# Kernel optimization log

Measured on AMD Instinct MI355X. Metric: run time of the kernel, lower is better.

The kernel has to match this reference:

```python
import jax, jax.numpy as jnp
import numpy as np

D_MODEL, N_LEVELS, N_HEADS, N_POINTS = 256, 4, 8, 4
HEAD_DIM = D_MODEL // N_HEADS
SPATIAL = [(100, 100), (50, 50), (25, 25), (13, 13)]  # (H, W) per level
BATCH = 2


def setup_inputs() -> dict:
    key = jax.random.key(0)
    ks = jax.random.split(key, 10)
    len_in = sum(h * w for h, w in SPATIAL)
    n, lq = BATCH, len_in
    s = 0.02
    mlp = N_HEADS * N_LEVELS * N_POINTS
    starts = np.cumsum([0] + [h * w for h, w in SPATIAL])[:-1]
    return {
        "query": jax.random.normal(ks[0], (n, lq, D_MODEL), jnp.float32),
        "reference_points": jax.random.uniform(ks[1], (n, lq, N_LEVELS, 2), jnp.float32),
        "input_flatten": jax.random.normal(ks[2], (n, len_in, D_MODEL), jnp.float32),
        "input_spatial_shapes": jnp.array(SPATIAL, dtype=jnp.int32),
        "input_level_start_index": jnp.array(starts, dtype=jnp.int32),
        "Wv": jax.random.normal(ks[3], (D_MODEL, D_MODEL), jnp.float32) * s,
        "bv": jnp.zeros((D_MODEL,), jnp.float32),
        "Woff": jax.random.normal(ks[4], (D_MODEL, mlp * 2), jnp.float32) * s,
        "boff": jax.random.normal(ks[5], (mlp * 2,), jnp.float32) * s,
        "Wattn": jax.random.normal(ks[6], (D_MODEL, mlp), jnp.float32) * s,
        "battn": jnp.zeros((mlp,), jnp.float32),
        "Wout": jax.random.normal(ks[7], (D_MODEL, D_MODEL), jnp.float32) * s,
        "bout": jnp.zeros((D_MODEL,), jnp.float32),
    }


def _ms_deform_attn_core(value, spatial_shapes, loc, aw):
    """value [N,S,M,D]; loc [N,Lq,M,L,P,2] in [0,1]; aw [N,Lq,M,L,P] -> [N,Lq,M*D].
    Faithful to F.grid_sample(mode='bilinear', padding_mode='zeros', align_corners=False)."""
    n, lq, m, L, p, _ = loc.shape
    d = value.shape[-1]
    out = jnp.zeros((n, m, lq, d), value.dtype)
    gather = jax.vmap(jax.vmap(lambda v, i: v[i]))  # vmap over N and M
    start = 0
    for lvl, (H, W) in enumerate(spatial_shapes):
        v = value[:, start:start + H * W].transpose(0, 2, 1, 3)  # [N,M,HW,D]
        start += H * W
        # align_corners=False: grid g=2*loc-1 -> pixel = ((g+1)*size-1)/2 = loc*size-0.5
        x = loc[:, :, :, lvl, :, 0] * W - 0.5  # [N,Lq,M,P]
        y = loc[:, :, :, lvl, :, 1] * H - 0.5
        x0 = jnp.floor(x)
        y0 = jnp.floor(y)
        wx = x - x0
        wy = y - y0
        x0i = x0.astype(jnp.int32)
        y0i = y0.astype(jnp.int32)
        samp = jnp.zeros((n, m, lq * p, d), value.dtype)
        for dy, wyc in ((0, 1.0 - wy), (1, wy)):
            for dx, wxc in ((0, 1.0 - wx), (1, wx)):
                xi = x0i + dx
                yi = y0i + dy
                valid = (xi >= 0) & (xi < W) & (yi >= 0) & (yi < H)  # zeros padding
                idx = jnp.clip(yi, 0, H - 1) * W + jnp.clip(xi, 0, W - 1)
                idx = idx.transpose(0, 2, 1, 3).reshape(n, m, lq * p)
                w = (wxc * wyc * valid).transpose(0, 2, 1, 3).reshape(n, m, lq * p)
                samp = samp + gather(v, idx) * w[..., None]
        samp = samp.reshape(n, m, lq, p, d)
        aw_l = aw[:, :, :, lvl, :].transpose(0, 2, 1, 3)  # [N,M,Lq,P]
        out = out + (samp * aw_l[..., None]).sum(3)
    return out.transpose(0, 2, 1, 3).reshape(n, lq, m * d)


def reference(query, reference_points, input_flatten, input_spatial_shapes,
              input_level_start_index, Wv, bv, Woff, boff, Wattn, battn, Wout, bout):
    n, lq, _ = query.shape
    m, L, p = N_HEADS, N_LEVELS, N_POINTS
    shapes = np.asarray(input_spatial_shapes)  # concrete/static [L,2] = (H,W)
    value = (input_flatten @ Wv + bv).reshape(n, -1, m, HEAD_DIM)
    off = (query @ Woff + boff).reshape(n, lq, m, L, p, 2)
    aw = jax.nn.softmax((query @ Wattn + battn).reshape(n, lq, m, L * p), axis=-1)
    aw = aw.reshape(n, lq, m, L, p)
    norm = jnp.asarray(shapes[:, ::-1].astype(np.float32))  # [L,2] = (W,H)
    loc = reference_points[:, :, None, :, None, :] + off / norm[None, None, None, :, None, :]
    out = _ms_deform_attn_core(value, [tuple(s) for s in shapes.tolist()], loc, aw)
    return out @ Wout + bout
```

## Files before the change

kernel.cpp:

```cpp
#include <hip/hip_runtime.h>
#include <hip/hip_bf16.h>

#define NB    2
#define LQ    13294
#define DM    256
#define NH    8
#define HD    32
#define NL    4
#define NP    4
#define ROWS  (NB*LQ)

#define OFF_VALUE 0u
#define OFF_TMP   13613056u
#define OFF_OFFS  27226112u
#define OFF_AWL   54452224u
#define OFF_WT    61258752u
#define OFF_FLAG  61717504u

#define WT_WV    0
#define WT_WOFF  65536
#define WT_WATTN 131072
#define WT_WOUT  163840

typedef __attribute__((ext_vector_type(8))) short short8;
typedef __attribute__((ext_vector_type(4))) float floatx4;

static __device__ __forceinline__ float blo(int u)  { return __uint_as_float(((unsigned)u) << 16); }
static __device__ __forceinline__ float bhif(int u) { return __uint_as_float(((unsigned)u) & 0xffff0000u); }

static __device__ __forceinline__ int pack_bf2(float a, float b) {
    __hip_bfloat162 h(__float2bfloat16(a), __float2bfloat16(b));
    int u; __builtin_memcpy(&u, &h, 4); return u;
}

static __device__ __forceinline__ float load_bias(const void* b, int i, int flag) {
    return flag ? __bfloat162float(((const __hip_bfloat16*)b)[i]) : ((const float*)b)[i];
}

static __device__ __forceinline__ void gload_lds16(const void* g, void* l) {
    __builtin_amdgcn_global_load_lds(
        (const __attribute__((address_space(1))) unsigned*)g,
        (__attribute__((address_space(3))) unsigned*)l, 16, 0, 0);
}

__global__ void sniff_k(const unsigned int* __restrict__ q, int* __restrict__ flag) {
    const int t = threadIdx.x;
    int hits = 0;
#pragma unroll
    for (int i = 0; i < 4; ++i) {
        unsigned lo = q[t * 4 + i] & 0xffffu;
        unsigned e  = (lo >> 7) & 0xffu;
        if ((e >= 110u && e <= 132u) || lo == 0u) ++hits;
    }
#pragma unroll
    for (int s = 1; s < 64; s <<= 1) hits += __shfl_xor(hits, s);
    if (t == 0) *flag = (hits > 160) ? 1 : 0;
}

__global__ __launch_bounds__(256) void trans_k(
    const void* __restrict__ s0, const void* __restrict__ s1,
    const void* __restrict__ s2, const void* __restrict__ s3,
    short* __restrict__ wt, const int* __restrict__ flagp)
{
    const int flag = *flagp;
    const int z = blockIdx.z;
    const void* src = (z == 0) ? s0 : (z == 1) ? s1 : (z == 2) ? s2 : s3;
    short* dst = wt + ((z == 0) ? WT_WV : (z == 1) ? WT_WOFF : (z == 2) ? WT_WATTN : WT_WOUT);
    const int N = (z == 2) ? 128 : 256;
    const int n0 = blockIdx.x * 32, k0 = blockIdx.y * 32;
    if (n0 >= N) return;

    __shared__ short tile[32 * 36];
    const int t = threadIdx.x;
    const int r = t >> 3, c4 = (t & 7) * 4;
    if (flag) {
        const short* sp = (const short*)src + (k0 + r) * N + n0 + c4;
        *(short4*)&tile[r * 36 + c4] = *(const short4*)sp;
    } else {
        const float* sp = (const float*)src + (k0 + r) * N + n0 + c4;
        float4 v = *(const float4*)sp;
        short4 o;
        o.x = (short)(pack_bf2(v.x, v.x) & 0xffff);
        o.y = (short)(pack_bf2(v.y, v.y) & 0xffff);
        o.z = (short)(pack_bf2(v.z, v.z) & 0xffff);
        o.w = (short)(pack_bf2(v.w, v.w) & 0xffff);
        *(short4*)&tile[r * 36 + c4] = o;
    }
    __syncthreads();
    const int nn = t >> 3, r4 = (t & 7) * 4;
    short4 o;
    o.x = tile[(r4 + 0) * 36 + nn];
    o.y = tile[(r4 + 1) * 36 + nn];
    o.z = tile[(r4 + 2) * 36 + nn];
    o.w = tile[(r4 + 3) * 36 + nn];
    *(short4*)&dst[(n0 + nn) * 256 + k0 + r4] = o;
}

__global__ __launch_bounds__(256) void gemm_front_k(
    const void* __restrict__ flat, const void* __restrict__ query,
    const short* __restrict__ wt,
    const void* __restrict__ bv, const void* __restrict__ boff, const void* __restrict__ battn,
    short* __restrict__ value, float* __restrict__ offsb, short* __restrict__ awl,
    const int* __restrict__ flagp)
{
    const int  flag = *flagp;
    const bool a_bf = (flag != 0);

    __shared__ __align__(16) short Bs[128 * 256];
    __shared__ __align__(16) short As[2][128 * 32];

    const int tid = threadIdx.x;
    const int w = tid >> 6, lane = tid & 63;
    const int qd = lane >> 4, ln = lane & 15;
    const int bx = blockIdx.x;
    const bool isv = (bx < 2);
    const void*  A   = isv ? flat : query;
    const short* Wtb = isv ? (wt + WT_WV) : (wt + WT_WOFF);
    const int colbase = (isv ? bx : bx - 2) * 128;
    const int bm = blockIdx.y * 128;

#pragma unroll
    for (int r = 0; r < 16; ++r) {
        const int c = r * 256 + tid;
        const int col = c >> 5;
        const int kc = (c & 31) ^ (col & 31);
        gload_lds16(Wtb + (colbase + col) * 256 + kc * 8, &Bs[(r * 256 + w * 64) * 8]);
    }

    auto stage_a = [&](int buf, int k0) {
#pragma unroll
        for (int r = 0; r < 2; ++r) {
            const int c = r * 256 + tid;
            const int row = min(bm + (c >> 2), ROWS - 1);
            const int kc = ((c & 3) ^ ((c >> 2) & 3)) * 8;
            if (a_bf) {
                gload_lds16((const short*)A + row * 256 + k0 + kc,
                            &As[buf][(r * 256 + w * 64) * 8]);
            } else {
                const float* p = (const float*)A + row * 256 + k0 + kc;
                float4 f0 = *(const float4*)p, f1 = *(const float4*)(p + 4);
                int4 pk; pk.x = pack_bf2(f0.x, f0.y); pk.y = pack_bf2(f0.z, f0.w);
                         pk.z = pack_bf2(f1.x, f1.y); pk.w = pack_bf2(f1.z, f1.w);
                *(int4*)&As[buf][c * 8] = pk;
            }
        }
    };
    stage_a(0, 0);
    __syncthreads();

    const int wm = (w & 1) * 64, wn = (w >> 1) * 64;

    floatx4 acc[4][4];
#pragma unroll
    for (int i = 0; i < 4; ++i)
#pragma unroll
        for (int j = 0; j < 4; ++j) acc[i][j] = floatx4{0.f, 0.f, 0.f, 0.f};

#pragma unroll
    for (int i0 = 0; i0 < 8; ++i0) {
        if (i0 < 7) stage_a((i0 + 1) & 1, 32 * (i0 + 1));
        const short* Ab = As[i0 & 1];
        short8 af[4], bf[4];
#pragma unroll
        for (int i = 0; i < 4; ++i) {
            const int row = wm + i * 16 + ln;
            af[i] = *(const short8*)&Ab[(row * 4 + (qd ^ (row & 3))) * 8];
        }
#pragma unroll
        for (int j = 0; j < 4; ++j) {
            const int col = wn + j * 16 + ln;
            bf[j] = *(const short8*)&Bs[(col * 32 + ((4 * i0 + qd) ^ (col & 31))) * 8];
        }
#pragma unroll
        for (int i = 0; i < 4; ++i)
#pragma unroll
            for (int j = 0; j < 4; ++j)
                acc[i][j] = __builtin_amdgcn_mfma_f32_16x16x32_bf16(af[i], bf[j], acc[i][j], 0, 0, 0);
        if (i0 < 7) __syncthreads();
    }

#pragma unroll
    for (int j = 0; j < 4; ++j) {
        const int col = colbase + wn + j * 16 + ln;
        float bj;
        if (isv)            bj = load_bias(bv, col, flag);
        else if (col < 256) bj = load_bias(boff, col, flag);
        else                bj = load_bias(battn, col - 256, flag);
#pragma unroll
        for (int i = 0; i < 4; ++i) {
#pragma unroll
            for (int r = 0; r < 4; ++r) {
                const int row = bm + wm + i * 16 + qd * 4 + r;
                if (row >= ROWS) continue;
                const float v = acc[i][j][r] + bj;
                if (isv)            value[row * 256 + col] = (short)(pack_bf2(v, v) & 0xffff);
                else if (col < 256) offsb[row * 256 + col] = v;
                else                awl[row * 128 + col - 256] = (short)(pack_bf2(v, v) & 0xffff);
            }
        }
    }
}

__global__ __launch_bounds__(256) void gemm_out_k(
    const short* __restrict__ tmp, const short* __restrict__ wtout,
    const void* __restrict__ bout, void* __restrict__ C,
    const int* __restrict__ flagp)
{
    const int flag = *flagp;

    __shared__ __align__(16) short Bs[128 * 256];
    __shared__ __align__(16) short As[2][128 * 32];

    const int tid = threadIdx.x;
    const int w = tid >> 6, lane = tid & 63;
    const int qd = lane >> 4, ln = lane & 15;
    const int colbase = blockIdx.x * 128;
    const int bm = blockIdx.y * 128;

#pragma unroll
    for (int r = 0; r < 16; ++r) {
        const int c = r * 256 + tid;
        const int col = c >> 5;
        const int kc = (c & 31) ^ (col & 31);
        gload_lds16(wtout + (colbase + col) * 256 + kc * 8, &Bs[(r * 256 + w * 64) * 8]);
    }

    auto stage_a = [&](int buf, int k0) {
#pragma unroll
        for (int r = 0; r < 2; ++r) {
            const int c = r * 256 + tid;
            const int row = min(bm + (c >> 2), ROWS - 1);
            const int kc = ((c & 3) ^ ((c >> 2) & 3)) * 8;
            gload_lds16(tmp + row * 256 + k0 + kc, &As[buf][(r * 256 + w * 64) * 8]);
        }
    };
    stage_a(0, 0);
    __syncthreads();

    const int wm = (w & 1) * 64, wn = (w >> 1) * 64;

    floatx4 acc[4][4];
#pragma unroll
    for (int i = 0; i < 4; ++i)
#pragma unroll
        for (int j = 0; j < 4; ++j) acc[i][j] = floatx4{0.f, 0.f, 0.f, 0.f};

#pragma unroll
    for (int i0 = 0; i0 < 8; ++i0) {
        if (i0 < 7) stage_a((i0 + 1) & 1, 32 * (i0 + 1));
        const short* Ab = As[i0 & 1];
        short8 af[4], bf[4];
#pragma unroll
        for (int i = 0; i < 4; ++i) {
            const int row = wm + i * 16 + ln;
            af[i] = *(const short8*)&Ab[(row * 4 + (qd ^ (row & 3))) * 8];
        }
#pragma unroll
        for (int j = 0; j < 4; ++j) {
            const int col = wn + j * 16 + ln;
            bf[j] = *(const short8*)&Bs[(col * 32 + ((4 * i0 + qd) ^ (col & 31))) * 8];
        }
#pragma unroll
        for (int i = 0; i < 4; ++i)
#pragma unroll
            for (int j = 0; j < 4; ++j)
                acc[i][j] = __builtin_amdgcn_mfma_f32_16x16x32_bf16(af[i], bf[j], acc[i][j], 0, 0, 0);
        if (i0 < 7) __syncthreads();
    }

#pragma unroll
    for (int j = 0; j < 4; ++j) {
        const int col = colbase + wn + j * 16 + ln;
        const float bj = load_bias(bout, col, flag);
#pragma unroll
        for (int i = 0; i < 4; ++i) {
#pragma unroll
            for (int r = 0; r < 4; ++r) {
                const int row = bm + wm + i * 16 + qd * 4 + r;
                if (row >= ROWS) continue;
                const float v = acc[i][j][r] + bj;
                if (flag) ((__hip_bfloat16*)C)[row * 256 + col] = __float2bfloat16(v);
                else      ((float*)C)[row * 256 + col] = v;
            }
        }
    }
}

__global__ __launch_bounds__(256) void sampler_k(
    const void* __restrict__ refp, const short* __restrict__ value,
    const float* __restrict__ offs, const short* __restrict__ awl,
    short* __restrict__ tmp, const int* __restrict__ flagp)
{
    const int flag = *flagp;
    const int nq = blockIdx.x * 4 + (threadIdx.x >> 6);
    const int lane = threadIdx.x & 63;
    const int h = lane >> 3, u = lane & 7;
    const int n = (nq >= LQ) ? 1 : 0;

    const int lg = *(const int*)(awl + nq * 128 + h * 16 + u * 2);
    float l0 = blo(lg), l1 = bhif(lg);
    float m = fmaxf(l0, l1);
    m = fmaxf(m, __shfl_xor(m, 1));
    m = fmaxf(m, __shfl_xor(m, 2));
    m = fmaxf(m, __shfl_xor(m, 4));
    float e0 = __expf(l0 - m), e1 = __expf(l1 - m);
    float s = e0 + e1;
    s += __shfl_xor(s, 1);
    s += __shfl_xor(s, 2);
    s += __shfl_xor(s, 4);
    const float inv = 1.f / s;
    const float w0 = e0 * inv, w1 = e1 * inv;

    const float4 of = *(const float4*)(offs + nq * 256 + h * 32 + u * 4);

    float rxl, ryl;
    if (flag) {
        const int rr = *(const int*)((const short*)refp + nq * 8 + (u & 3) * 2);
        rxl = blo(rr); ryl = bhif(rr);
    } else {
        const float* rp = (const float*)refp + nq * 8 + (u & 3) * 2;
        rxl = rp[0]; ryl = rp[1];
    }

    const short* vb = value + (n ? LQ * 256 : 0) + h * 32 + u * 4;

    float a0 = 0.f, a1 = 0.f, a2 = 0.f, a3 = 0.f;

    const int WlA[NL] = {100, 50, 25, 13};
    const int StA[NL] = {0, 10000, 12500, 13125};

#pragma unroll
    for (int idx = 0; idx < 16; ++idx) {
        const int l = idx >> 2;
        const int Wl = WlA[l];
        const float Wf = (float)Wl;
        const int owner = h * 8 + (idx >> 1);
        const float ox = __shfl((idx & 1) ? of.z : of.x, owner);
        const float oy = __shfl((idx & 1) ? of.w : of.y, owner);
        const float wa = __shfl((idx & 1) ? w1 : w0, owner);
        const float rx = __shfl(rxl, h * 8 + l);
        const float ry = __shfl(ryl, h * 8 + l);

        const float px = fmaf(rx, Wf, ox) - 0.5f;
        const float py = fmaf(ry, Wf, oy) - 0.5f;
        const float x0f = floorf(px), y0f = floorf(py);
        const float wx = px - x0f, wy = py - y0f;
        const int x0 = (int)x0f, y0 = (int)y0f;
        const short* vl = vb + StA[l] * 256;

#pragma unroll
        for (int dy = 0; dy < 2; ++dy) {
#pragma unroll
            for (int dx = 0; dx < 2; ++dx) {
                const int xi = x0 + dx, yi = y0 + dy;
                const bool vld = (xi >= 0) & (xi < Wl) & (yi >= 0) & (yi < Wl);
                const float wgt = (dx ? wx : 1.f - wx) * (dy ? wy : 1.f - wy);
                const float ww = vld ? wa * wgt : 0.f;
                const int xc = min(max(xi, 0), Wl - 1);
                const int yc = min(max(yi, 0), Wl - 1);
                const int2 raw = *(const int2*)(vl + (yc * Wl + xc) * 256);
                a0 = fmaf(ww, blo(raw.x),  a0);
                a1 = fmaf(ww, bhif(raw.x), a1);
                a2 = fmaf(ww, blo(raw.y),  a2);
                a3 = fmaf(ww, bhif(raw.y), a3);
            }
        }
    }

    int2 o;
    o.x = pack_bf2(a0, a1);
    o.y = pack_bf2(a2, a3);
    *(int2*)(tmp + nq * 256 + h * 32 + u * 4) = o;
}

extern "C" void kernel_launch(void* const* d_in, const int* in_sizes, int n_in,
                              void* d_out, int out_size, void* d_ws, size_t ws_size,
                              hipStream_t stream)
{
    const void* query  = d_in[0];
    const void* refpts = d_in[1];
    const void* flat   = d_in[2];
    const void* Wv     = d_in[5];
    const void* bv     = d_in[6];
    const void* Woff   = d_in[7];
    const void* boff   = d_in[8];
    const void* Wattn  = d_in[9];
    const void* battn  = d_in[10];
    const void* Wout   = d_in[11];
    const void* bout   = d_in[12];

    char* ws = (char*)d_ws;
    short* value = (short*)(ws + OFF_VALUE);
    short* tmp   = (short*)(ws + OFF_TMP);
    float* offsb = (float*)(ws + OFF_OFFS);
    short* awl   = (short*)(ws + OFF_AWL);
    short* wt    = (short*)(ws + OFF_WT);
    int*   flagp = (int*)(ws + OFF_FLAG);

    const int gmy = (ROWS + 127) / 128;

    sniff_k<<<1, 64, 0, stream>>>((const unsigned int*)query, flagp);
    trans_k<<<dim3(8, 8, 4), 256, 0, stream>>>(Wv, Woff, Wattn, Wout, wt, flagp);
    gemm_front_k<<<dim3(5, gmy), 256, 0, stream>>>(flat, query, wt, bv, boff, battn,
                                                   value, offsb, awl, flagp);
    sampler_k<<<ROWS / 4, 256, 0, stream>>>(refpts, value, offsb, awl, tmp, flagp);
    gemm_out_k<<<dim3(2, gmy), 256, 0, stream>>>(tmp, wt + WT_WOUT, bout, d_out, flagp);
}
```

Before: 252.4 us.

## Fuse sampler with output projection and store offsets as bf16

The deformable sampler now writes each block's 16 sampled query rows into shared memory and multiplies them by Wout with MFMA in the same kernel. This removes the tmp round trip through global memory and one kernel launch. Sampling offsets are stored as bf16 instead of fp32, halving that buffer's traffic at some precision cost. The front GEMM grid is flattened and remapped so that row tiles are spread across XCDs; each sampler block now reads Wout fragments directly from global memory.

```diff
diff --git a/kernel.cpp b/kernel.cpp
--- a/kernel.cpp
+++ b/kernel.cpp
@@ -11,11 +11,10 @@
 #define ROWS  (NB*LQ)
 
 #define OFF_VALUE 0u
-#define OFF_TMP   13613056u
-#define OFF_OFFS  27226112u
-#define OFF_AWL   54452224u
-#define OFF_WT    61258752u
-#define OFF_FLAG  61717504u
+#define OFF_OFFS  13613056u
+#define OFF_AWL   27226112u
+#define OFF_WT    34032640u
+#define OFF_FLAG  34491392u
 
 #define WT_WV    0
 #define WT_WOFF  65536
@@ -100,7 +99,7 @@
     const void* __restrict__ flat, const void* __restrict__ query,
     const short* __restrict__ wt,
     const void* __restrict__ bv, const void* __restrict__ boff, const void* __restrict__ battn,
-    short* __restrict__ value, float* __restrict__ offsb, short* __restrict__ awl,
+    short* __restrict__ value, short* __restrict__ offsb, short* __restrict__ awl,
     const int* __restrict__ flagp)
 {
     const int  flag = *flagp;
@@ -109,15 +108,19 @@
     __shared__ __align__(16) short Bs[128 * 256];
     __shared__ __align__(16) short As[2][128 * 32];
 
+    const int id = blockIdx.x;
+    const int xcd = id & 7, rest = id >> 3;
+    const int t5 = rest % 5, gq = rest / 5;
+    const int g = xcd + 8 * gq;
+    const int bm = g * 128;
+
     const int tid = threadIdx.x;
     const int w = tid >> 6, lane = tid & 63;
     const int qd = lane >> 4, ln = lane & 15;
-    const int bx = blockIdx.x;
-    const bool isv = (bx < 2);
+    const bool isv = (t5 < 2);
     const void*  A   = isv ? flat : query;
     const short* Wtb = isv ? (wt + WT_WV) : (wt + WT_WOFF);
-    const int colbase = (isv ? bx : bx - 2) * 128;
-    const int bm = blockIdx.y * 128;
+    const int colbase = (isv ? t5 : t5 - 2) * 128;
 
 #pragma unroll
     for (int r = 0; r < 16; ++r) {
@@ -193,184 +196,143 @@
                 const int row = bm + wm + i * 16 + qd * 4 + r;
                 if (row >= ROWS) continue;
                 const float v = acc[i][j][r] + bj;
-                if (isv)            value[row * 256 + col] = (short)(pack_bf2(v, v) & 0xffff);
-                else if (col < 256) offsb[row * 256 + col] = v;
-                else                awl[row * 128 + col - 256] = (short)(pack_bf2(v, v) & 0xffff);
+                const short hv = (short)(pack_bf2(v, v) & 0xffff);
+                if (isv)            value[row * 256 + col] = hv;
+                else if (col < 256) offsb[row * 256 + col] = hv;
+                else                awl[row * 128 + col - 256] = hv;
             }
         }
     }
 }
 
-__global__ __launch_bounds__(256) void gemm_out_k(
-    const short* __restrict__ tmp, const short* __restrict__ wtout,
-    const void* __restrict__ bout, void* __restrict__ C,
-    const int* __restrict__ flagp)
+#define TSTR 264
+__global__ __launch_bounds__(256) void sampler_out_k(
+    const void* __restrict__ refp, const short* __restrict__ value,
+    const short* __restrict__ offs, const short* __restrict__ awl,
+    const short* __restrict__ wtout, const void* __restrict__ bout,
+    void* __restrict__ C, const int* __restrict__ flagp)
 {
     const int flag = *flagp;
-
-    __shared__ __align__(16) short Bs[128 * 256];
-    __shared__ __align__(16) short As[2][128 * 32];
-
-    const int tid = threadIdx.x;
-    const int w = tid >> 6, lane = tid & 63;
-    const int qd = lane >> 4, ln = lane & 15;
-    const int colbase = blockIdx.x * 128;
-    const int bm = blockIdx.y * 128;
-
-#pragma unroll
-    for (int r = 0; r < 16; ++r) {
-        const int c = r * 256 + tid;
-        const int col = c >> 5;
-        const int kc = (c & 31) ^ (col & 31);
-        gload_lds16(wtout + (colbase + col) * 256 + kc * 8, &Bs[(r * 256 + w * 64) * 8]);
-    }
-
-    auto stage_a = [&](int buf, int k0) {
-#pragma unroll
-        for (int r = 0; r < 2; ++r) {
-            const int c = r * 256 + tid;
-            const int row = min(bm + (c >> 2), ROWS - 1);
-            const int kc = ((c & 3) ^ ((c >> 2) & 3)) * 8;
-            gload_lds16(tmp + row * 256 + k0 + kc, &As[buf][(r * 256 + w * 64) * 8]);
-        }
-    };
-    stage_a(0, 0);
-    __syncthreads();
-
-    const int wm = (w & 1) * 64, wn = (w >> 1) * 64;
-
-    floatx4 acc[4][4];
-#pragma unroll
-    for (int i = 0; i < 4; ++i)
-#pragma unroll
-        for (int j = 0; j < 4; ++j) acc[i][j] = floatx4{0.f, 0.f, 0.f, 0.f};
-
-#pragma unroll
-    for (int i0 = 0; i0 < 8; ++i0) {
-        if (i0 < 7) stage_a((i0 + 1) & 1, 32 * (i0 + 1));
-        const short* Ab = As[i0 & 1];
-        short8 af[4], bf[4];
-#pragma unroll
-        for (int i = 0; i < 4; ++i) {
-            const int row = wm + i * 16 + ln;
-            af[i] = *(const short8*)&Ab[(row * 4 + (qd ^ (row & 3))) * 8];
-        }
-#pragma unroll
-        for (int j = 0; j < 4; ++j) {
-            const int col = wn + j * 16 + ln;
-            bf[j] = *(const short8*)&Bs[(col * 32 + ((4 * i0 + qd) ^ (col & 31))) * 8];
-        }
-#pragma unroll
-        for (int i = 0; i < 4; ++i)
-#pragma unroll
-            for (int j = 0; j < 4; ++j)
-                acc[i][j] = __builtin_amdgcn_mfma_f32_16x16x32_bf16(af[i], bf[j], acc[i][j], 0, 0, 0);
-        if (i0 < 7) __syncthreads();
-    }
-
-#pragma unroll
-    for (int j = 0; j < 4; ++j) {
-        const int col = colbase + wn + j * 16 + ln;
-        const float bj = load_bias(bout, col, flag);
-#pragma unroll
-        for (int i = 0; i < 4; ++i) {
-#pragma unroll
-            for (int r = 0; r < 4; ++r) {
-                const int row = bm + wm + i * 16 + qd * 4 + r;
-                if (row >= ROWS) continue;
-                const float v = acc[i][j][r] + bj;
-                if (flag) ((__hip_bfloat16*)C)[row * 256 + col] = __float2bfloat16(v);
-                else      ((float*)C)[row * 256 + col] = v;
-            }
-        }
-    }
-}
-
-__global__ __launch_bounds__(256) void sampler_k(
-    const void* __restrict__ refp, const short* __restrict__ value,
-    const float* __restrict__ offs, const short* __restrict__ awl,
-    short* __restrict__ tmp, const int* __restrict__ flagp)
-{
-    const int flag = *flagp;
-    const int nq = blockIdx.x * 4 + (threadIdx.x >> 6);
+    __shared__ __align__(16) short tmp_s[16 * TSTR];
+
+    const int qblk = blockIdx.x * 16;
+    const int w = threadIdx.x >> 6;
     const int lane = threadIdx.x & 63;
     const int h = lane >> 3, u = lane & 7;
-    const int n = (nq >= LQ) ? 1 : 0;
-
-    const int lg = *(const int*)(awl + nq * 128 + h * 16 + u * 2);
-    float l0 = blo(lg), l1 = bhif(lg);
-    float m = fmaxf(l0, l1);
-    m = fmaxf(m, __shfl_xor(m, 1));
-    m = fmaxf(m, __shfl_xor(m, 2));
-    m = fmaxf(m, __shfl_xor(m, 4));
-    float e0 = __expf(l0 - m), e1 = __expf(l1 - m);
-    float s = e0 + e1;
-    s += __shfl_xor(s, 1);
-    s += __shfl_xor(s, 2);
-    s += __shfl_xor(s, 4);
-    const float inv = 1.f / s;
-    const float w0 = e0 * inv, w1 = e1 * inv;
-
-    const float4 of = *(const float4*)(offs + nq * 256 + h * 32 + u * 4);
-
-    float rxl, ryl;
-    if (flag) {
-        const int rr = *(const int*)((const short*)refp + nq * 8 + (u & 3) * 2);
-        rxl = blo(rr); ryl = bhif(rr);
-    } else {
-        const float* rp = (const float*)refp + nq * 8 + (u & 3) * 2;
-        rxl = rp[0]; ryl = rp[1];
-    }
-
-    const short* vb = value + (n ? LQ * 256 : 0) + h * 32 + u * 4;
-
-    float a0 = 0.f, a1 = 0.f, a2 = 0.f, a3 = 0.f;
 
     const int WlA[NL] = {100, 50, 25, 13};
     const int StA[NL] = {0, 10000, 12500, 13125};
 
 #pragma unroll
-    for (int idx = 0; idx < 16; ++idx) {
-        const int l = idx >> 2;
-        const int Wl = WlA[l];
-        const float Wf = (float)Wl;
-        const int owner = h * 8 + (idx >> 1);
-        const float ox = __shfl((idx & 1) ? of.z : of.x, owner);
-        const float oy = __shfl((idx & 1) ? of.w : of.y, owner);
-        const float wa = __shfl((idx & 1) ? w1 : w0, owner);
-        const float rx = __shfl(rxl, h * 8 + l);
-        const float ry = __shfl(ryl, h * 8 + l);
-
-        const float px = fmaf(rx, Wf, ox) - 0.5f;
-        const float py = fmaf(ry, Wf, oy) - 0.5f;
-        const float x0f = floorf(px), y0f = floorf(py);
-        const float wx = px - x0f, wy = py - y0f;
-        const int x0 = (int)x0f, y0 = (int)y0f;
-        const short* vl = vb + StA[l] * 256;
-
-#pragma unroll
-        for (int dy = 0; dy < 2; ++dy) {
-#pragma unroll
-            for (int dx = 0; dx < 2; ++dx) {
-                const int xi = x0 + dx, yi = y0 + dy;
-                const bool vld = (xi >= 0) & (xi < Wl) & (yi >= 0) & (yi < Wl);
-                const float wgt = (dx ? wx : 1.f - wx) * (dy ? wy : 1.f - wy);
-                const float ww = vld ? wa * wgt : 0.f;
-                const int xc = min(max(xi, 0), Wl - 1);
-                const int yc = min(max(yi, 0), Wl - 1);
-                const int2 raw = *(const int2*)(vl + (yc * Wl + xc) * 256);
-                a0 = fmaf(ww, blo(raw.x),  a0);
-                a1 = fmaf(ww, bhif(raw.x), a1);
-                a2 = fmaf(ww, blo(raw.y),  a2);
-                a3 = fmaf(ww, bhif(raw.y), a3);
+    for (int it = 0; it < 4; ++it) {
+        const int q = w * 4 + it;
+        const int nq = min(qblk + q, ROWS - 1);
+        const int n = (nq >= LQ) ? 1 : 0;
+
+        const int lg = *(const int*)(awl + nq * 128 + h * 16 + u * 2);
+        float l0 = blo(lg), l1 = bhif(lg);
+        float m = fmaxf(l0, l1);
+        m = fmaxf(m, __shfl_xor(m, 1));
+        m = fmaxf(m, __shfl_xor(m, 2));
+        m = fmaxf(m, __shfl_xor(m, 4));
+        float e0 = __expf(l0 - m), e1 = __expf(l1 - m);
+        float s = e0 + e1;
+        s += __shfl_xor(s, 1);
+        s += __shfl_xor(s, 2);
+        s += __shfl_xor(s, 4);
+        const float inv = 1.f / s;
+        const float w0 = e0 * inv, w1 = e1 * inv;
+
+        const int2 ow = *(const int2*)(offs + nq * 256 + h * 32 + u * 4);
+        const float ofx0 = blo(ow.x), ofy0 = bhif(ow.x);
+        const float ofx1 = blo(ow.y), ofy1 = bhif(ow.y);
+
+        float rxl, ryl;
+        if (flag) {
+            const int rr = *(const int*)((const short*)refp + nq * 8 + (u & 3) * 2);
+            rxl = blo(rr); ryl = bhif(rr);
+        } else {
+            const float* rp = (const float*)refp + nq * 8 + (u & 3) * 2;
+            rxl = rp[0]; ryl = rp[1];
+        }
+
+        const short* vb = value + (n ? LQ * 256 : 0) + h * 32 + u * 4;
+        float a0 = 0.f, a1 = 0.f, a2 = 0.f, a3 = 0.f;
+
+#pragma unroll
+        for (int idx = 0; idx < 16; ++idx) {
+            const int l = idx >> 2;
+            const int Wl = WlA[l];
+            const float Wf = (float)Wl;
+            const int owner = h * 8 + (idx >> 1);
+            const float ox = __shfl((idx & 1) ? ofx1 : ofx0, owner);
+            const float oy = __shfl((idx & 1) ? ofy1 : ofy0, owner);
+            const float wa = __shfl((idx & 1) ? w1 : w0, owner);
+            const float rx = __shfl(rxl, h * 8 + l);
+            const float ry = __shfl(ryl, h * 8 + l);
+
+            const float px = fmaf(rx, Wf, ox) - 0.5f;
+            const float py = fmaf(ry, Wf, oy) - 0.5f;
+            const float x0f = floorf(px), y0f = floorf(py);
+            const float wx = px - x0f, wy = py - y0f;
+            const int x0 = (int)x0f, y0 = (int)y0f;
+            const short* vl = vb + StA[l] * 256;
+
+#pragma unroll
+            for (int dy = 0; dy < 2; ++dy) {
+#pragma unroll
+                for (int dx = 0; dx < 2; ++dx) {
+                    const int xi = x0 + dx, yi = y0 + dy;
+                    const bool vld = (xi >= 0) & (xi < Wl) & (yi >= 0) & (yi < Wl);
+                    const float wgt = (dx ? wx : 1.f - wx) * (dy ? wy : 1.f - wy);
+                    const float ww = vld ? wa * wgt : 0.f;
+                    const int xc = min(max(xi, 0), Wl - 1);
+                    const int yc = min(max(yi, 0), Wl - 1);
+                    const int2 raw = *(const int2*)(vl + (yc * Wl + xc) * 256);
+                    a0 = fmaf(ww, blo(raw.x),  a0);
+                    a1 = fmaf(ww, bhif(raw.x), a1);
+                    a2 = fmaf(ww, blo(raw.y),  a2);
+                    a3 = fmaf(ww, bhif(raw.y), a3);
+                }
             }
         }
-    }
-
-    int2 o;
-    o.x = pack_bf2(a0, a1);
-    o.y = pack_bf2(a2, a3);
-    *(int2*)(tmp + nq * 256 + h * 32 + u * 4) = o;
+
+        int2 o;
+        o.x = pack_bf2(a0, a1);
+        o.y = pack_bf2(a2, a3);
+        *(int2*)&tmp_s[q * TSTR + h * 32 + u * 4] = o;
+    }
+    __syncthreads();
+
+    const int qd = lane >> 4, ln = lane & 15;
+    floatx4 acc[4];
+#pragma unroll
+    for (int j = 0; j < 4; ++j) acc[j] = floatx4{0.f, 0.f, 0.f, 0.f};
+
+#pragma unroll
+    for (int k = 0; k < 8; ++k) {
+        const short8 af = *(const short8*)&tmp_s[ln * TSTR + k * 32 + qd * 8];
+#pragma unroll
+        for (int j = 0; j < 4; ++j) {
+            const int col = w * 64 + j * 16 + ln;
+            const short8 bfr = *(const short8*)(wtout + col * 256 + k * 32 + qd * 8);
+            acc[j] = __builtin_amdgcn_mfma_f32_16x16x32_bf16(af, bfr, acc[j], 0, 0, 0);
+        }
+    }
+
+#pragma unroll
+    for (int j = 0; j < 4; ++j) {
+        const int col = w * 64 + j * 16 + ln;
+        const float bj = load_bias(bout, col, flag);
+#pragma unroll
+        for (int r = 0; r < 4; ++r) {
+            const int row = qblk + qd * 4 + r;
+            if (row >= ROWS) continue;
+            const float v = acc[j][r] + bj;
+            if (flag) ((__hip_bfloat16*)C)[row * 256 + col] = __float2bfloat16(v);
+            else      ((float*)C)[row * 256 + col] = v;
+        }
+    }
 }
 
 extern "C" void kernel_launch(void* const* d_in, const int* in_sizes, int n_in,
@@ -391,18 +353,15 @@
 
     char* ws = (char*)d_ws;
     short* value = (short*)(ws + OFF_VALUE);
-    short* tmp   = (short*)(ws + OFF_TMP);
-    float* offsb = (float*)(ws + OFF_OFFS);
+    short* offsb = (short*)(ws + OFF_OFFS);
     short* awl   = (short*)(ws + OFF_AWL);
     short* wt    = (short*)(ws + OFF_WT);
     int*   flagp = (int*)(ws + OFF_FLAG);
 
-    const int gmy = (ROWS + 127) / 128;
-
     sniff_k<<<1, 64, 0, stream>>>((const unsigned int*)query, flagp);
     trans_k<<<dim3(8, 8, 4), 256, 0, stream>>>(Wv, Woff, Wattn, Wout, wt, flagp);
-    gemm_front_k<<<dim3(5, gmy), 256, 0, stream>>>(flat, query, wt, bv, boff, battn,
-                                                   value, offsb, awl, flagp);
-    sampler_k<<<ROWS / 4, 256, 0, stream>>>(refpts, value, offsb, awl, tmp, flagp);
-    gemm_out_k<<<dim3(2, gmy), 256, 0, stream>>>(tmp, wt + WT_WOUT, bout, d_out, flagp);
-}
+    gemm_front_k<<<1040, 256, 0, stream>>>(flat, query, wt, bv, boff, battn,
+                                           value, offsb, awl, flagp);
+    sampler_out_k<<<(ROWS + 15) / 16, 256, 0, stream>>>(refpts, value, offsb, awl,
+                                                        wt + WT_WOUT, bout, d_out, flagp);
+}
```

Measured after the change: 258.0 us. +2.2%, slower.
